# Kernel optimization log

Measured on AMD Instinct MI355X. Metric: run time of the kernel, lower is better.

The kernel has to match this reference:

```python
import jax, jax.numpy as jnp
import numpy as np

B, L, D, H, K = 4, 4096, 1024, 16, 256

def setup_inputs() -> dict:
    key = jax.random.key(0)
    ks = jax.random.split(key, 11)
    s = 0.02
    return {
        "x": jax.random.normal(ks[0], (B, L, D), jnp.float32),
        "Wq": jax.random.normal(ks[1], (D, D), jnp.float32) * s,
        "bq": jax.random.normal(ks[2], (D,), jnp.float32) * s,
        "Wk": jax.random.normal(ks[3], (D, D), jnp.float32) * s,
        "bk": jax.random.normal(ks[4], (D,), jnp.float32) * s,
        "Wv": jax.random.normal(ks[5], (D, D), jnp.float32) * s,
        "bv": jax.random.normal(ks[6], (D,), jnp.float32) * s,
        "E": jax.random.normal(ks[7], (L, K), jnp.float32),
        "F": jax.random.normal(ks[8], (L, K), jnp.float32),
        "Wo": jax.random.normal(ks[9], (D, D), jnp.float32) * s,
        "bo": jax.random.normal(ks[10], (D,), jnp.float32) * s,
        "n_heads": H,
    }

def reference(x, Wq, bq, Wk, bk, Wv, bv, E, F, Wo, bo, n_heads):
    Bc, Lc, Dc = x.shape
    hd = Dc // n_heads
    scale = hd ** -0.5
    # QKV projections (torch Linear: x @ W.T + b; here W stored as [in,out])
    q = (x @ Wq + bq).reshape(Bc, Lc, n_heads, hd)  # blhd
    k = (x @ Wk + bk).reshape(Bc, Lc, n_heads, hd)
    v = (x @ Wv + bv).reshape(Bc, Lc, n_heads, hd)
    # Low-rank projection of K/V sequence dim: L -> K
    kE = jnp.einsum('blhd,lk->bhkd', k, E[:Lc])
    vF = jnp.einsum('blhd,lk->bhkd', v, F[:Lc])
    # Attention over compressed dim k
    qk = jnp.einsum('blhd,bhkd->bhlk', q, kE) * scale
    attn = jax.nn.softmax(qk, axis=-1)
    out = jnp.einsum('bhlk,bhkd->blhd', attn, vF).reshape(Bc, Lc, Dc)
    return out @ Wo + bo
```

## Files before the change

### kernel.cpp

```cpp
#include <hip/hip_runtime.h>

typedef _Float16 half_t;
typedef __attribute__((ext_vector_type(8))) _Float16 f16x8;
typedef __attribute__((ext_vector_type(4))) _Float16 f16x4;
typedef __attribute__((ext_vector_type(4))) float f32x4;
typedef __attribute__((ext_vector_type(4))) float float4v;

__device__ __forceinline__ void gload_lds16(const void* g, void* l) {
  __builtin_amdgcn_global_load_lds(
      (const __attribute__((address_space(1))) void*)g,
      (__attribute__((address_space(3))) void*)l, 16, 0, 0);
}

template<int OUTMODE>
__global__ __launch_bounds__(512, 2)
void gemm_big(const half_t* __restrict__ A, const half_t* __restrict__ Bt,
              void* __restrict__ Cv, const float* __restrict__ bias, float alpha)
{
  __shared__ __attribute__((aligned(16))) char lds[131072];
  const int tid = threadIdx.x, w = tid >> 6, lane = tid & 63;
  const int wr = w >> 2, wc = w & 3;
  const int g = lane >> 4, cc = lane & 15;
  const int m0 = blockIdx.x * 256, n0 = blockIdx.y * 256;

  const int srow2 = tid >> 2, sslot = tid & 3;
  const int swslot = sslot ^ ((srow2 >> 1) & 3);
  const int swr = (g ^ ((cc >> 1) & 3)) << 4;

  const f32x4 zero = {0.f, 0.f, 0.f, 0.f};
  f32x4 acc[8][4];
#pragma unroll
  for (int i = 0; i < 8; ++i)
#pragma unroll
    for (int j = 0; j < 4; ++j) acc[i][j] = zero;

  auto STAGE_HALF = [&](int ktile, int hh, char* sb) {
    const int kk = hh >> 1, isB = hh & 1;
    const half_t* src = isB ? Bt : A;
    const int base_row = isB ? n0 : m0;
    const long rowoff = (long)(base_row + srow2) * 1024 + ktile * 64 + kk * 32 + swslot * 8;
    char* d = sb + isB * 32768 + kk * 16384;
    gload_lds16(src + rowoff,          d + tid * 16);
    gload_lds16(src + rowoff + 131072, d + 8192 + tid * 16);
  };

  {
    char* b0 = lds;
    STAGE_HALF(0, 0, b0); STAGE_HALF(0, 1, b0);
    STAGE_HALF(0, 2, b0); STAGE_HALF(0, 3, b0);
  }
  asm volatile("s_waitcnt vmcnt(4)" ::: "memory");
  __builtin_amdgcn_s_barrier();

#pragma unroll 1
  for (int n = 0; n < 16; ++n) {
    const char* rb = lds + ((n & 1) << 16);
    char* sb = lds + (((n + 1) & 1) << 16);
    f16x8 bf[4];
#pragma unroll
    for (int ph = 0; ph < 4; ++ph) {
      const int kk = ph >> 1, fh = ph & 1;
      f16x8 af[4];
      const char* Ah = rb + kk * 16384;
#pragma unroll
      for (int mf = 0; mf < 4; ++mf)
        af[mf] = *(const f16x8*)(Ah + (wr * 128 + fh * 64 + mf * 16 + cc) * 64 + swr);
      if (fh == 0) {
        const char* Bh = rb + 32768 + kk * 16384;
#pragma unroll
        for (int nf = 0; nf < 4; ++nf)
          bf[nf] = *(const f16x8*)(Bh + (wc * 64 + nf * 16 + cc) * 64 + swr);
      }
      if (n < 15) STAGE_HALF(n + 1, ph, sb);
      __builtin_amdgcn_sched_barrier(0);
      __builtin_amdgcn_s_barrier();
      asm volatile("s_waitcnt lgkmcnt(0)" ::: "memory");
      __builtin_amdgcn_sched_barrier(0);
      __builtin_amdgcn_s_setprio(1);
#pragma unroll
      for (int mf = 0; mf < 4; ++mf)
#pragma unroll
        for (int nf = 0; nf < 4; ++nf)
          acc[fh * 4 + mf][nf] =
              __builtin_amdgcn_mfma_f32_16x16x32_f16(af[mf], bf[nf], acc[fh * 4 + mf][nf], 0, 0, 0);
      __builtin_amdgcn_s_setprio(0);
      __builtin_amdgcn_sched_barrier(0);
      if (ph == 1) {
        if (n < 15) { asm volatile("s_waitcnt vmcnt(4)" ::: "memory"); }
        else        { asm volatile("s_waitcnt vmcnt(0)" ::: "memory"); }
      } else if (ph == 3) {
        if (n < 15) { asm volatile("s_waitcnt vmcnt(4)" ::: "memory"); }
      }
      __builtin_amdgcn_s_barrier();
    }
  }

#pragma unroll
  for (int mf = 0; mf < 8; ++mf)
#pragma unroll
    for (int nf = 0; nf < 4; ++nf)
#pragma unroll
      for (int r = 0; r < 4; ++r) {
        const int row = m0 + wr * 128 + mf * 16 + g * 4 + r;
        const int col = n0 + wc * 64 + nf * 16 + cc;
        float v = (acc[mf][nf][r] + bias[col]) * alpha;
        if (OUTMODE == 0) {
          ((float*)Cv)[(long)row * 1024 + col] = v;
        } else {
          const int bb = row >> 12, l = row & 4095, h = col >> 6, d = col & 63;
          ((half_t*)Cv)[(((long)(bb * 16 + h) * 4096 + l) << 6) + d] = (half_t)v;
        }
      }
}

template<int SK>
__global__ __launch_bounds__(256, 2)
void gemm_xef(const half_t* __restrict__ A, const half_t* __restrict__ Bt,
              float* __restrict__ Cv, int lda, int ldb, long sB, long sC)
{
  __shared__ __attribute__((aligned(16))) half_t As[128 * 32];
  __shared__ __attribute__((aligned(16))) half_t Bs[128 * 32];

  const int tid = threadIdx.x, w = tid >> 6, lane = tid & 63;
  const int wr = w >> 1, wc = w & 1;
  const int z = blockIdx.z / SK, ks = blockIdx.z % SK;
  const half_t* Ab = A;
  const half_t* Bb = Bt + (long)z * sB;
  const int m0 = blockIdx.x * 128, n0 = blockIdx.y * 128;
  const int g = lane >> 4, cc = lane & 15;
  const int srow = lane >> 2, scol = (lane & 3) * 8;

  const f32x4 zero = {0.f, 0.f, 0.f, 0.f};
  f32x4 acc[4][4];
#pragma unroll
  for (int i = 0; i < 4; ++i)
#pragma unroll
    for (int j = 0; j < 4; ++j) acc[i][j] = zero;

  const int kchunk = 4096 / SK;
  for (int kt = ks * kchunk; kt < (ks + 1) * kchunk; kt += 32) {
#pragma unroll
    for (int j = 0; j < 2; ++j) {
      const int bi = w * 2 + j;
      gload_lds16(Ab + (long)(m0 + bi * 16 + srow) * lda + kt + scol, &As[bi * 512]);
      gload_lds16(Bb + (long)(n0 + bi * 16 + srow) * ldb + kt + scol, &Bs[bi * 512]);
    }
    __syncthreads();

    f16x8 af[4], bf[4];
#pragma unroll
    for (int i = 0; i < 4; ++i)
      af[i] = *(const f16x8*)&As[(wr * 64 + i * 16 + cc) * 32 + g * 8];
#pragma unroll
    for (int j = 0; j < 4; ++j)
      bf[j] = *(const f16x8*)&Bs[(wc * 64 + j * 16 + cc) * 32 + g * 8];
#pragma unroll
    for (int i = 0; i < 4; ++i)
#pragma unroll
      for (int j = 0; j < 4; ++j)
        acc[i][j] = __builtin_amdgcn_mfma_f32_16x16x32_f16(af[i], bf[j], acc[i][j], 0, 0, 0);
    __syncthreads();
  }

  const int nb = gridDim.z / SK;
#pragma unroll
  for (int i = 0; i < 4; ++i)
#pragma unroll
    for (int j = 0; j < 4; ++j)
#pragma unroll
      for (int r = 0; r < 4; ++r) {
        const int row = m0 + wr * 64 + i * 16 + g * 4 + r;
        const int col = n0 + wc * 64 + j * 16 + cc;
        Cv[((long)ks * nb + z) * sC + (long)row * 1024 + col] = acc[i][j][r];
      }
}

__global__ __launch_bounds__(256, 2)
void gemm_kevf(const half_t* __restrict__ xEF, const half_t* __restrict__ Wkt,
               const half_t* __restrict__ Wvt, half_t* __restrict__ kEb,
               half_t* __restrict__ vFtb, const float* __restrict__ bk,
               const float* __restrict__ bv, const float* __restrict__ sEF)
{
  __shared__ __attribute__((aligned(16))) half_t As[64 * 32];
  __shared__ __attribute__((aligned(16))) half_t Bs[64 * 32];
  const int tid = threadIdx.x, w = tid >> 6, lane = tid & 63;
  const int wr = w >> 1, wc = w & 1;
  const int g = lane >> 4, cc = lane & 15;
  const int srow = lane >> 2, scol = (lane & 3) * 8;

  const int bid = blockIdx.x;
  const int role = bid >> 8, lb = bid & 255;
  const half_t *Ap, *Bp;
  int m0, n0, z;
  if (role == 0) {
    m0 = (lb & 3) * 64; n0 = ((lb >> 2) & 15) * 64; z = lb >> 6;
    Ap = xEF + (long)z * 524288;  Bp = Wkt;
  } else {
    m0 = (lb & 15) * 64; n0 = ((lb >> 4) & 3) * 64; z = lb >> 6;
    Ap = Wvt;  Bp = xEF + (long)z * 524288 + 262144;
  }

  const f32x4 zero = {0.f, 0.f, 0.f, 0.f};
  f32x4 acc[2][2];
#pragma unroll
  for (int i = 0; i < 2; ++i)
#pragma unroll
    for (int j = 0; j < 2; ++j) acc[i][j] = zero;

  for (int kt = 0; kt < 1024; kt += 32) {
    gload_lds16(Ap + (long)(m0 + w * 16 + srow) * 1024 + kt + scol, &As[w * 512]);
    gload_lds16(Bp + (long)(n0 + w * 16 + srow) * 1024 + kt + scol, &Bs[w * 512]);
    __syncthreads();
    f16x8 af[2], bf[2];
#pragma unroll
    for (int i = 0; i < 2; ++i)
      af[i] = *(const f16x8*)&As[(wr * 32 + i * 16 + cc) * 32 + g * 8];
#pragma unroll
    for (int j = 0; j < 2; ++j)
      bf[j] = *(const f16x8*)&Bs[(wc * 32 + j * 16 + cc) * 32 + g * 8];
#pragma unroll
    for (int i = 0; i < 2; ++i)
#pragma unroll
      for (int j = 0; j < 2; ++j)
        acc[i][j] = __builtin_amdgcn_mfma_f32_16x16x32_f16(af[i], bf[j], acc[i][j], 0, 0, 0);
    __syncthreads();
  }

#pragma unroll
  for (int i = 0; i < 2; ++i)
#pragma unroll
    for (int j = 0; j < 2; ++j)
#pragma unroll
      for (int r = 0; r < 4; ++r) {
        const int row = m0 + wr * 32 + i * 16 + g * 4 + r;
        const int col = n0 + wc * 32 + j * 16 + cc;
        float v = acc[i][j][r];
        if (role == 0) {
          v += sEF[row] * bk[col];
          kEb[(long)z * 262144 + (long)(col >> 6) * 16384 + (long)row * 64 + (col & 63)]
              = (half_t)v;
        } else {
          v += bv[row] * sEF[256 + col];
          vFtb[(long)z * 262144 + (long)row * 256 + col] = (half_t)v;
        }
      }
}

__global__ __launch_bounds__(512, 2)
void attn_fused(const half_t* __restrict__ qhb, const half_t* __restrict__ kEh,
                const half_t* __restrict__ vFt, half_t* __restrict__ outp, int L)
{
  __shared__ __attribute__((aligned(16))) half_t Ks[256 * 64];
  __shared__ __attribute__((aligned(16))) half_t Vs[64 * 256];
  const int tid = threadIdx.x, w = tid >> 6, lane = tid & 63;
  const int g = lane >> 4, c = lane & 15;
  const int l0 = blockIdx.x * 256, h = blockIdx.y, b = blockIdx.z;

  const half_t* keh = kEh + (long)(b * 16 + h) * 16384;
  const half_t* vfh = vFt + (long)b * 262144 + (long)h * 16384;
  const half_t* qpan = qhb + ((long)(b * 16 + h) * 4096 + l0) * 64;
  half_t* ob = outp + ((long)b * L + l0 + w * 32) * 1024 + h * 64;

#pragma unroll
  for (int i = 0; i < 4; ++i) {
    const int row = i * 64 + (tid >> 3), slot = tid & 7;
    gload_lds16(qpan + row * 64 + ((slot ^ (row & 7)) << 3),
                (char*)Ks + i * 8192 + tid * 16);
  }
#pragma unroll
  for (int i = 0; i < 4; ++i) {
    const int row = i * 16 + (tid >> 5), slot = tid & 31;
    gload_lds16(vfh + row * 256 + ((slot ^ (row & 7)) << 3),
                (char*)Vs + i * 8192 + tid * 16);
  }
  __syncthreads();

  f16x8 qf[2][2];
#pragma unroll
  for (int fi = 0; fi < 2; ++fi) {
    const int qrow = w * 32 + fi * 16 + c;
    const char* qp = (const char*)Ks + qrow * 128;
#pragma unroll
    for (int ks = 0; ks < 2; ++ks)
      qf[fi][ks] = *(const f16x8*)(qp + (((ks * 4 + g) ^ (qrow & 7)) << 4));
  }
  __syncthreads();

#pragma unroll
  for (int i = 0; i < 4; ++i) {
    const int row = i * 64 + (tid >> 3), slot = tid & 7;
    gload_lds16(keh + row * 64 + ((slot ^ (row & 7)) << 3),
                (char*)Ks + i * 8192 + tid * 16);
  }
  __syncthreads();

  const f32x4 zero = {0.f, 0.f, 0.f, 0.f};
  f32x4 o[2][4];
#pragma unroll
  for (int fi = 0; fi < 2; ++fi)
#pragma unroll
    for (int fd = 0; fd < 4; ++fd) o[fi][fd] = zero;
  float mrun[2] = {-3.0e38f, -3.0e38f};
  float lrun[2] = {0.f, 0.f};

  for (int ch = 0; ch < 4; ++ch) {
    f32x4 s[2][4];
#pragma unroll
    for (int fi = 0; fi < 2; ++fi)
#pragma unroll
      for (int fj = 0; fj < 4; ++fj) s[fi][fj] = zero;
#pragma unroll
    for (int fj = 0; fj < 4; ++fj) {
      const int krow = ch * 64 + fj * 16 + c;
      const char* kb = (const char*)Ks + krow * 128;
      f16x8 k0 = *(const f16x8*)(kb + ((g ^ (c & 7)) << 4));
      f16x8 k1 = *(const f16x8*)(kb + (((4 + g) ^ (c & 7)) << 4));
#pragma unroll
      for (int fi = 0; fi < 2; ++fi) {
        s[fi][fj] = __builtin_amdgcn_mfma_f32_16x16x32_f16(k0, qf[fi][0], s[fi][fj], 0, 0, 0);
        s[fi][fj] = __builtin_amdgcn_mfma_f32_16x16x32_f16(k1, qf[fi][1], s[fi][fj], 0, 0, 0);
      }
    }

    f16x4 p[2][4];
#pragma unroll
    for (int fi = 0; fi < 2; ++fi) {
      float cm = -3.0e38f;
#pragma unroll
      for (int fj = 0; fj < 4; ++fj)
#pragma unroll
        for (int r = 0; r < 4; ++r) cm = fmaxf(cm, s[fi][fj][r]);
      cm = fmaxf(cm, __shfl_xor(cm, 16));
      cm = fmaxf(cm, __shfl_xor(cm, 32));
      const float mref = mrun[fi];
      const bool keep = __all(cm - mref <= 8.0f);
      const float mnew = keep ? mref : fmaxf(mref, cm);
      float csum = 0.f;
#pragma unroll
      for (int fj = 0; fj < 4; ++fj) {
        f16x4 fr;
#pragma unroll
        for (int r = 0; r < 4; ++r) {
          float e = __expf(s[fi][fj][r] - mnew);
          fr[r] = (half_t)e; csum += e;
        }
        p[fi][fj] = fr;
      }
      csum += __shfl_xor(csum, 16);
      csum += __shfl_xor(csum, 32);
      if (keep) {
        lrun[fi] += csum;
      } else {
        const float sc = __expf(mref - mnew);
        lrun[fi] = lrun[fi] * sc + csum;
        mrun[fi] = mnew;
#pragma unroll
        for (int fd = 0; fd < 4; ++fd)
#pragma unroll
          for (int r = 0; r < 4; ++r) o[fi][fd][r] *= sc;
      }
    }

#pragma unroll
    for (int kc = 0; kc < 4; ++kc) {
      const int s16 = ch * 8 + kc * 2 + (g >> 1);
      f16x4 va[4];
#pragma unroll
      for (int fd = 0; fd < 4; ++fd) {
        const int drow = fd * 16 + c;
        va[fd] = *(const f16x4*)((const char*)Vs + drow * 512 +
                                 ((s16 ^ (c & 7)) << 4) + (g & 1) * 8);
      }
#pragma unroll
      for (int fi = 0; fi < 2; ++fi)
#pragma unroll
        for (int fd = 0; fd < 4; ++fd)
          o[fi][fd] = __builtin_amdgcn_mfma_f32_16x16x16f16(va[fd], p[fi][kc], o[fi][fd], 0, 0, 0);
    }
  }

#pragma unroll
  for (int fi = 0; fi < 2; ++fi) {
    const float inv = 1.0f / lrun[fi];
#pragma unroll
    for (int fd = 0; fd < 4; ++fd) {
      f16x4 st;
#pragma unroll
      for (int r = 0; r < 4; ++r) st[r] = (half_t)(o[fi][fd][r] * inv);
      *(f16x4*)(ob + (long)(fi * 16 + c) * 1024 + fd * 16 + g * 4) = st;
    }
  }
}

__global__ __launch_bounds__(256, 4)
void prepass(const float* __restrict__ x, half_t* __restrict__ xhf,
             half_t* __restrict__ xT,
             const float* __restrict__ E, const float* __restrict__ F,
             half_t* __restrict__ EFt, float* __restrict__ sEF,
             const float* __restrict__ Wq, const float* __restrict__ Wk,
             const float* __restrict__ Wv, const float* __restrict__ Wo,
             half_t* __restrict__ Wqt, half_t* __restrict__ Wkt,
             half_t* __restrict__ Wvt, half_t* __restrict__ Wot)
{
  __shared__ float t[32][33];
  __shared__ float ps[8][32];
  const int tx = threadIdx.x, ty = threadIdx.y;
  const int id = blockIdx.x;

  if (id < 16384) {
    const int bx = id & 31, by = (id >> 5) & 127, bz = id >> 12;
    const int d0 = bx * 32, l0 = by * 32;
    const float* ip = x + ((long)bz * 4096 + l0) * 1024 + d0;
    half_t* oh = xhf + ((long)bz * 4096 + l0) * 1024 + d0;
#pragma unroll
    for (int j = 0; j < 4; ++j) {
      float v = ip[(long)(ty + 8 * j) * 1024 + tx];
      t[ty + 8 * j][tx] = v;
      oh[(long)(ty + 8 * j) * 1024 + tx] = (half_t)v;
    }
    __syncthreads();
    half_t* ot = xT + ((long)bz * 1024 + d0) * 4096 + l0;
#pragma unroll
    for (int j = 0; j < 4; ++j)
      ot[(long)(ty + 8 * j) * 4096 + tx] = (half_t)t[tx][ty + 8 * j];
  } else if (id < 18432) {
    const int id2 = id - 16384;
    const int bx = id2 & 7, by = (id2 >> 3) & 127, zz = id2 >> 10;
    const float* in = zz ? F : E;
    half_t* oT = EFt + (long)zz * 1048576;
    float* sm = sEF + zz * 256;
    const int k0 = bx * 32, l0 = by * 32;
    float p = 0.f;
#pragma unroll
    for (int j = 0; j < 4; ++j) {
      float v = in[(long)(l0 + ty + 8 * j) * 256 + k0 + tx];
      t[ty + 8 * j][tx] = v; p += v;
    }
    ps[ty][tx] = p;
    __syncthreads();
    if (ty == 0) {
      float a = 0.f;
#pragma unroll
      for (int r = 0; r < 8; ++r) a += ps[r][tx];
      atomicAdd(&sm[k0 + tx], a);
    }
#pragma unroll
    for (int j = 0; j < 4; ++j)
      oT[(long)(k0 + ty + 8 * j) * 4096 + l0 + tx] = (half_t)t[tx][ty + 8 * j];
  } else {
    const int id3 = id - 18432;
    const int bx = id3 & 31, by = (id3 >> 5) & 31, zz = id3 >> 10;
    const float* in = (zz == 0) ? Wq : (zz == 1) ? Wk : (zz == 2) ? Wv : Wo;
    half_t* out = (zz == 0) ? Wqt : (zz == 1) ? Wkt : (zz == 2) ? Wvt : Wot;
    const int cx = bx * 32 + tx, r0 = by * 32;
#pragma unroll
    for (int j = 0; j < 4; ++j)
      t[ty + 8 * j][tx] = in[(long)(r0 + ty + 8 * j) * 1024 + cx];
    __syncthreads();
    const int rx = r0 + tx, cy = bx * 32 + ty;
#pragma unroll
    for (int j = 0; j < 4; ++j)
      out[(long)(cy + 8 * j) * 1024 + rx] = (half_t)t[tx][ty + 8 * j];
  }
}

__global__ void reduce4_f16(const float* __restrict__ in, half_t* __restrict__ out) {
  long i = ((long)blockIdx.x * 256 + threadIdx.x) * 4;
  float4v a = *(const float4v*)(in + i);
#pragma unroll
  for (int ks = 1; ks < 4; ++ks) {
    float4v t = *(const float4v*)(in + (long)ks * 2097152 + i);
    a.x += t.x; a.y += t.y; a.z += t.z; a.w += t.w;
  }
  f16x4 o;
  o[0] = (half_t)a.x; o[1] = (half_t)a.y; o[2] = (half_t)a.z; o[3] = (half_t)a.w;
  *(f16x4*)(out + i) = o;
}

extern "C" void kernel_launch(void* const* d_in, const int* in_sizes, int n_in,
                              void* d_out, int out_size, void* d_ws, size_t ws_size,
                              hipStream_t stream)
{
  const float* x  = (const float*)d_in[0];
  const float* Wq = (const float*)d_in[1];
  const float* bq = (const float*)d_in[2];
  const float* Wk = (const float*)d_in[3];
  const float* bk = (const float*)d_in[4];
  const float* Wv = (const float*)d_in[5];
  const float* bv = (const float*)d_in[6];
  const float* E  = (const float*)d_in[7];
  const float* F  = (const float*)d_in[8];
  const float* Wo = (const float*)d_in[9];
  const float* bo = (const float*)d_in[10];
  float* out = (float*)d_out;

  char* ws = (char*)d_ws;
  half_t* xhf  = (half_t*)(ws);
  half_t* xT   = (half_t*)(ws + 33554432);
  half_t* qhf  = (half_t*)(ws + 67108864);
  half_t* Wqt  = (half_t*)(ws + 100663296);
  half_t* Wkt  = Wqt + 1048576;
  half_t* Wvt  = Wkt + 1048576;
  half_t* Wot  = Wvt + 1048576;
  half_t* EFt  = (half_t*)(ws + 109051904);
  half_t* xEF  = (half_t*)(ws + 113246208);
  half_t* kEb  = (half_t*)(ws + 117440512);
  half_t* vFtb = (half_t*)(ws + 119537664);
  float*  sEF  = (float*)(ws + 121634816);
  half_t* outp = xhf;
  float*  xEFf = (float*)d_out;

  hipMemsetAsync(sEF, 0, 2048, stream);
  prepass<<<dim3(22528), dim3(32, 8), 0, stream>>>(
      x, xhf, xT, E, F, EFt, sEF, Wq, Wk, Wv, Wo, Wqt, Wkt, Wvt, Wot);

  gemm_xef<4><<<dim3(4, 8, 16), 256, 0, stream>>>(
      EFt, xT, xEFf, 4096, 4096, 4194304, 524288);
  reduce4_f16<<<2048, 256, 0, stream>>>(xEFf, xEF);

  gemm_big<2><<<dim3(64, 4), 512, 0, stream>>>(xhf, Wqt, qhf, bq, 0.125f);
  gemm_kevf<<<dim3(512), 256, 0, stream>>>(xEF, Wkt, Wvt, kEb, vFtb, bk, bv, sEF);
  attn_fused<<<dim3(16, 16, 4), 512, 0, stream>>>(qhf, kEb, vFtb, outp, 4096);
  gemm_big<0><<<dim3(64, 4), 512, 0, stream>>>(outp, Wot, (void*)out, bo, 1.0f);
  (void)bq; (void)in_sizes; (void)n_in; (void)out_size; (void)ws_size;
}
```

Before: 216.4 us.

## Load Q fragments directly from global and widen prepass transpose tiles to 64x64

The attention kernel now reads its Q fragments straight from global memory into registers instead of staging them through LDS. This removes one LDS round trip and two barriers, so the K and V LDS fills start right away. The prepass transpose/convert kernel moves from 32x32 to 64x64 tiles with 64x4 thread blocks, cutting the block count fourfold and widening the contiguous row segments each warp touches. The cost is uncoalesced-ish direct Q reads and higher LDS use per prepass block, which may lower occupancy.

Measured after the change: 213.8 us. About the same (-1.2%).

```diff
diff --git a/kernel.cpp b/kernel.cpp
--- a/kernel.cpp
+++ b/kernel.cpp
@@ -264,7 +264,7 @@
 #pragma unroll
   for (int i = 0; i < 4; ++i) {
     const int row = i * 64 + (tid >> 3), slot = tid & 7;
-    gload_lds16(qpan + row * 64 + ((slot ^ (row & 7)) << 3),
+    gload_lds16(keh + row * 64 + ((slot ^ (row & 7)) << 3),
                 (char*)Ks + i * 8192 + tid * 16);
   }
 #pragma unroll
@@ -273,25 +273,14 @@
     gload_lds16(vfh + row * 256 + ((slot ^ (row & 7)) << 3),
                 (char*)Vs + i * 8192 + tid * 16);
   }
-  __syncthreads();
 
   f16x8 qf[2][2];
 #pragma unroll
-  for (int fi = 0; fi < 2; ++fi) {
-    const int qrow = w * 32 + fi * 16 + c;
-    const char* qp = (const char*)Ks + qrow * 128;
+  for (int fi = 0; fi < 2; ++fi)
 #pragma unroll
     for (int ks = 0; ks < 2; ++ks)
-      qf[fi][ks] = *(const f16x8*)(qp + (((ks * 4 + g) ^ (qrow & 7)) << 4));
-  }
-  __syncthreads();
-
-#pragma unroll
-  for (int i = 0; i < 4; ++i) {
-    const int row = i * 64 + (tid >> 3), slot = tid & 7;
-    gload_lds16(keh + row * 64 + ((slot ^ (row & 7)) << 3),
-                (char*)Ks + i * 8192 + tid * 16);
-  }
+      qf[fi][ks] = *(const f16x8*)(qpan + (w * 32 + fi * 16 + c) * 64 + ks * 32 + g * 8);
+
   __syncthreads();
 
   const f32x4 zero = {0.f, 0.f, 0.f, 0.f};
@@ -402,65 +391,72 @@
              half_t* __restrict__ Wqt, half_t* __restrict__ Wkt,
              half_t* __restrict__ Wvt, half_t* __restrict__ Wot)
 {
-  __shared__ float t[32][33];
-  __shared__ float ps[8][32];
+  __shared__ float t[64][65];
+  __shared__ float ps[4][64];
   const int tx = threadIdx.x, ty = threadIdx.y;
   const int id = blockIdx.x;
 
-  if (id < 16384) {
-    const int bx = id & 31, by = (id >> 5) & 127, bz = id >> 12;
-    const int d0 = bx * 32, l0 = by * 32;
+  if (id < 4096) {
+    const int bx = id & 15, by = (id >> 4) & 63, bz = id >> 10;
+    const int d0 = bx * 64, l0 = by * 64;
     const float* ip = x + ((long)bz * 4096 + l0) * 1024 + d0;
     half_t* oh = xhf + ((long)bz * 4096 + l0) * 1024 + d0;
 #pragma unroll
-    for (int j = 0; j < 4; ++j) {
-      float v = ip[(long)(ty + 8 * j) * 1024 + tx];
-      t[ty + 8 * j][tx] = v;
-      oh[(long)(ty + 8 * j) * 1024 + tx] = (half_t)v;
+    for (int j = 0; j < 16; ++j) {
+      const int row = ty + 4 * j;
+      float v = ip[(long)row * 1024 + tx];
+      t[row][tx] = v;
+      oh[(long)row * 1024 + tx] = (half_t)v;
     }
     __syncthreads();
     half_t* ot = xT + ((long)bz * 1024 + d0) * 4096 + l0;
 #pragma unroll
-    for (int j = 0; j < 4; ++j)
-      ot[(long)(ty + 8 * j) * 4096 + tx] = (half_t)t[tx][ty + 8 * j];
-  } else if (id < 18432) {
-    const int id2 = id - 16384;
-    const int bx = id2 & 7, by = (id2 >> 3) & 127, zz = id2 >> 10;
+    for (int j = 0; j < 16; ++j) {
+      const int drow = ty + 4 * j;
+      ot[(long)drow * 4096 + tx] = (half_t)t[tx][drow];
+    }
+  } else if (id < 4608) {
+    const int id2 = id - 4096;
+    const int bx = id2 & 3, by = (id2 >> 2) & 63, zz = id2 >> 8;
     const float* in = zz ? F : E;
     half_t* oT = EFt + (long)zz * 1048576;
     float* sm = sEF + zz * 256;
-    const int k0 = bx * 32, l0 = by * 32;
+    const int k0 = bx * 64, l0 = by * 64;
     float p = 0.f;
 #pragma unroll
-    for (int j = 0; j < 4; ++j) {
-      float v = in[(long)(l0 + ty + 8 * j) * 256 + k0 + tx];
-      t[ty + 8 * j][tx] = v; p += v;
+    for (int j = 0; j < 16; ++j) {
+      const int row = ty + 4 * j;
+      float v = in[(long)(l0 + row) * 256 + k0 + tx];
+      t[row][tx] = v; p += v;
     }
     ps[ty][tx] = p;
     __syncthreads();
     if (ty == 0) {
-      float a = 0.f;
-#pragma unroll
-      for (int r = 0; r < 8; ++r) a += ps[r][tx];
+      float a = ps[0][tx] + ps[1][tx] + ps[2][tx] + ps[3][tx];
       atomicAdd(&sm[k0 + tx], a);
     }
 #pragma unroll
-    for (int j = 0; j < 4; ++j)
-      oT[(long)(k0 + ty + 8 * j) * 4096 + l0 + tx] = (half_t)t[tx][ty + 8 * j];
+    for (int j = 0; j < 16; ++j) {
+      const int krow = ty + 4 * j;
+      oT[(long)(k0 + krow) * 4096 + l0 + tx] = (half_t)t[tx][krow];
+    }
   } else {
-    const int id3 = id - 18432;
-    const int bx = id3 & 31, by = (id3 >> 5) & 31, zz = id3 >> 10;
+    const int id3 = id - 4608;
+    const int bx = id3 & 15, by = (id3 >> 4) & 15, zz = id3 >> 8;
     const float* in = (zz == 0) ? Wq : (zz == 1) ? Wk : (zz == 2) ? Wv : Wo;
     half_t* out = (zz == 0) ? Wqt : (zz == 1) ? Wkt : (zz == 2) ? Wvt : Wot;
-    const int cx = bx * 32 + tx, r0 = by * 32;
-#pragma unroll
-    for (int j = 0; j < 4; ++j)
-      t[ty + 8 * j][tx] = in[(long)(r0 + ty + 8 * j) * 1024 + cx];
-    __syncthreads();
-    const int rx = r0 + tx, cy = bx * 32 + ty;
-#pragma unroll
-    for (int j = 0; j < 4; ++j)
-      out[(long)(cy + 8 * j) * 1024 + rx] = (half_t)t[tx][ty + 8 * j];
+    const int c0 = bx * 64, r0 = by * 64;
+#pragma unroll
+    for (int j = 0; j < 16; ++j) {
+      const int row = ty + 4 * j;
+      t[row][tx] = in[(long)(r0 + row) * 1024 + c0 + tx];
+    }
+    __syncthreads();
+#pragma unroll
+    for (int j = 0; j < 16; ++j) {
+      const int crow = ty + 4 * j;
+      out[(long)(c0 + crow) * 1024 + r0 + tx] = (half_t)t[tx][crow];
+    }
   }
 }
 
@@ -511,7 +507,7 @@
   float*  xEFf = (float*)d_out;
 
   hipMemsetAsync(sEF, 0, 2048, stream);
-  prepass<<<dim3(22528), dim3(32, 8), 0, stream>>>(
+  prepass<<<dim3(5632), dim3(64, 4), 0, stream>>>(
       x, xhf, xT, E, F, EFt, sEF, Wq, Wk, Wv, Wo, Wqt, Wkt, Wvt, Wot);
 
   gemm_xef<4><<<dim3(4, 8, 16), 256, 0, stream>>>(
```
